# Kernel optimization log

Measured on AMD Instinct MI355X. Metric: run time of the kernel, lower is better.

The kernel has to match this reference:

```python
import jax, jax.numpy as jnp
import numpy as np

# Model constants (from module __init__ / repo script)
DT = 60                    # model time step [s]
DT_FORCING = 3600          # forcing time step [s]
NSUB = DT_FORCING // DT    # substeps between forcing samples = 60
NT = 5_040_000             # number of model steps (~9.6 years at dt=60s)
NF = NT // NSUB            # forcing series length = 84000
FC = 1e-4                  # Coriolis frequency


def setup_inputs() -> dict:
    key = jax.random.key(0)
    k1, k2, k3 = jax.random.split(key, 3)
    # pk = log(K); K ~ exp(-10) ~ 4.5e-5 keeps the Euler recurrence stable (|a|<1)
    pk = -10.0 + 0.1 * jax.random.normal(k1, (2,), dtype=jnp.float32)
    # wind stress forcing, around the repo's 0.2 N/m^2 zonal value
    TAx = 0.2 + 0.05 * jax.random.normal(k2, (NF,), dtype=jnp.float32)
    TAy = 0.05 * jax.random.normal(k3, (NF,), dtype=jnp.float32)
    return {"pk": pk, "TAx": TAx, "TAy": TAy}


def reference(pk, TAx, TAy):
    K = jnp.exp(pk)                                    # K[0]: wind coeff, K[1]: damping
    TA = TAx.astype(jnp.complex64) + 1j * TAy.astype(jnp.complex64)  # [NF]

    # Vectorized linear interpolation of forcing onto every model step it=0..NT-2
    it = jnp.arange(NT - 1)
    itf = it // NSUB
    aa = (it % NSUB).astype(jnp.float32) / NSUB
    # faithful to original: compares against NT (never true), then relies on
    # JAX's clamping gather for the final out-of-range itf+1
    itsup = jnp.where(itf + 1 >= NT, -1, itf + 1)
    TAi = (1.0 - aa) * TA[itf] + aa * TA[itsup]        # [NT-1] complex64

    # U_{t+1} = U_t + dt*(-i*fc*U_t + K0*TA_t - K1*U_t) = a*U_t + b_t
    a = jnp.asarray(1.0 + DT * (-1j * FC - K[1]), dtype=jnp.complex64)
    b = (DT * K[0]).astype(jnp.complex64) * TAi        # [NT-1]

    def step(u, bt):
        u_next = a * u + bt
        return u_next, u_next

    u0 = jnp.zeros((), dtype=jnp.complex64)
    _, ys = jax.lax.scan(step, u0, b)                  # [NT-1]
    U = jnp.concatenate([u0[None], ys])                # [NT], U[0] = 0
    return jnp.real(U), jnp.imag(U)
```

## Files before the change

kernel.cpp:

```cpp
#include <hip/hip_runtime.h>
#include <math.h>

#define NTOT   5040000
#define NFORC  84000
#define NSUB_  60
#define NSTEPS (NTOT - 1)

#define TPB     256
#define SEGS    60
#define WIN     (TPB * SEGS)
#define WARM    4800
#define CHUNK   (WIN - WARM)
#define TILE    30
#define TSTRIDE 31

__global__ __launch_bounds__(TPB, 2)
void slab_scan_kernel(const float* __restrict__ pk,
                      const float* __restrict__ TAx,
                      const float* __restrict__ TAy,
                      float* __restrict__ out)
{
    __shared__ float2 tb[TPB * TSTRIDE];

    const int tid = threadIdx.x;
    const int blk = blockIdx.x;

    const float K0 = expf(pk[0]);
    const float K1 = expf(pk[1]);
    const float ar = 1.0f - 60.0f * K1;
    const float ai = -60.0f * 1.0e-4f;
    const float s  = 60.0f * K0;

    const int wstart = blk * CHUNK;
    const int wend   = min(wstart + CHUNK, NSTEPS);
    const int ws     = max(0, wstart - WARM);

    const int itf = ws / NSUB_ + tid;
    const int i0  = min(itf,     NFORC - 1);
    const int i1  = min(itf + 1, NFORC - 1);
    const float x0 = TAx[i0], y0 = TAy[i0];
    const float x1 = TAx[i1], y1 = TAy[i1];
    const float cinv = s * (1.0f / 60.0f);
    const float dxs  = (x1 - x0) * cinv;
    const float dys  = (y1 - y0) * cinv;
    const float b0re = s * x0;
    const float b0im = s * y0;

    float ur = 0.f, ui = 0.f;
    {
        float bre = b0re, bim = b0im;
        #pragma unroll
        for (int k = 0; k < SEGS; ++k) {
            float nr = fmaf(ar, ur, fmaf(-ai, ui, bre));
            float ni = fmaf(ar, ui, fmaf( ai, ur, bim));
            ur = nr; ui = ni;
            bre += dxs; bim += dys;
        }
    }

    float2 apow[8];
    {
        double br_ = (double)ar, bi_ = (double)ai;
        double prr = 1.0, pii = 0.0;
        int e = SEGS;
        while (e) {
            if (e & 1) { double t = prr*br_ - pii*bi_; pii = prr*bi_ + pii*br_; prr = t; }
            double t = br_*br_ - bi_*bi_; bi_ = 2.0*br_*bi_; br_ = t;
            e >>= 1;
        }
        double cr = prr, ci = pii;
        #pragma unroll
        for (int k = 0; k < 8; ++k) {
            apow[k] = make_float2((float)cr, (float)ci);
            double t = cr*cr - ci*ci; ci = 2.0*cr*ci; cr = t;
        }
    }

    float2 v = make_float2(ur, ui);
    tb[tid] = v;
    __syncthreads();
    #pragma unroll
    for (int k = 0; k < 8; ++k) {
        const int off = 1 << k;
        float2 prev = make_float2(0.f, 0.f);
        if (tid >= off) prev = tb[tid - off];
        __syncthreads();
        v.x = fmaf(apow[k].x, prev.x, fmaf(-apow[k].y, prev.y, v.x));
        v.y = fmaf(apow[k].x, prev.y, fmaf( apow[k].y, prev.x, v.y));
        tb[tid] = v;
        __syncthreads();
    }
    float usr = 0.f, usi = 0.f;
    if (tid > 0) { float2 p = tb[tid - 1]; usr = p.x; usi = p.y; }
    __syncthreads();

    ur = usr; ui = usi;
    float bre = b0re, bim = b0im;
    for (int h = 0; h < SEGS / TILE; ++h) {
        #pragma unroll
        for (int k = 0; k < TILE; ++k) {
            float nr = fmaf(ar, ur, fmaf(-ai, ui, bre));
            float ni = fmaf(ar, ui, fmaf( ai, ur, bim));
            ur = nr; ui = ni;
            bre += dxs; bim += dys;
            tb[tid * TSTRIDE + k] = make_float2(nr, ni);
        }
        __syncthreads();
        {
            int row = tid / TILE;
            int k   = tid - row * TILE;
            for (int i = 0; i < TILE; ++i) {
                float2 w = tb[row * TSTRIDE + k];
                const int o = ws + row * SEGS + h * TILE + k;
                if (o >= wstart && o < wend) {
                    out[o + 1]        = w.x;
                    out[NTOT + o + 1] = w.y;
                }
                row += 8; k += 16;
                if (k >= TILE) { k -= TILE; row += 1; }
            }
        }
        __syncthreads();
    }

    if (blk == 0 && tid == 0) { out[0] = 0.f; out[NTOT] = 0.f; }
}

extern "C" void kernel_launch(void* const* d_in, const int* in_sizes, int n_in,
                              void* d_out, int out_size, void* d_ws, size_t ws_size,
                              hipStream_t stream)
{
    const float* pk  = (const float*)d_in[0];
    const float* TAx = (const float*)d_in[1];
    const float* TAy = (const float*)d_in[2];
    float* out = (float*)d_out;

    const int nblocks = (NSTEPS + CHUNK - 1) / CHUNK;
    slab_scan_kernel<<<dim3(nblocks), dim3(TPB), 0, stream>>>(pk, TAx, TAy, out);
}
```

Measured before the change: 78.31 us.

## Compute segment sums in closed form and use wave-shuffle scan with vector stores

Replaces the first sequential 60-step pass per thread with a closed-form segment contribution (G*b0 + H*db), where G and H are computed in double precision. The block-wide LDS scan, which needed many barriers, becomes a 64-lane shuffle scan plus a small cross-wave combine. The shared-memory transpose for output is dropped in favour of direct per-thread float4 stores, and launch bounds now allow 4 blocks per CU. This removes half of the serial recurrence work and most of the LDS traffic, at the cost of per-thread double-precision setup and strided, less coalesced global writes.

```diff
diff --git a/kernel.cpp b/kernel.cpp
--- a/kernel.cpp
+++ b/kernel.cpp
@@ -3,127 +3,156 @@
 
 #define NTOT   5040000
 #define NFORC  84000
-#define NSUB_  60
 #define NSTEPS (NTOT - 1)
 
-#define TPB     256
-#define SEGS    60
-#define WIN     (TPB * SEGS)
-#define WARM    4800
-#define CHUNK   (WIN - WARM)
-#define TILE    30
-#define TSTRIDE 31
+#define TPB    256
+#define SEGS   60
+#define WIN    (TPB * SEGS)
+#define WARM   4800
+#define CHUNK  (WIN - WARM)
+#define NBLK   ((NSTEPS + CHUNK - 1) / CHUNK)
 
-__global__ __launch_bounds__(TPB, 2)
-void slab_scan_kernel(const float* __restrict__ pk,
-                      const float* __restrict__ TAx,
-                      const float* __restrict__ TAy,
-                      float* __restrict__ out)
+struct cd { double x, y; };
+__device__ __forceinline__ cd cmuld(cd a, cd b){ return {a.x*b.x - a.y*b.y, a.x*b.y + a.y*b.x}; }
+__device__ __forceinline__ cd cdivd(cd a, cd b){
+    double r = 1.0 / (b.x*b.x + b.y*b.y);
+    return {(a.x*b.x + a.y*b.y)*r, (a.y*b.x - a.x*b.y)*r};
+}
+
+__device__ __forceinline__ float2 cfma(float2 m, float2 p, float2 v) {
+    v.x = fmaf(m.x, p.x, fmaf(-m.y, p.y, v.x));
+    v.y = fmaf(m.x, p.y, fmaf( m.y, p.x, v.y));
+    return v;
+}
+__device__ __forceinline__ float2 cmulf(float2 a, float2 b){
+    return make_float2(a.x*b.x - a.y*b.y, a.x*b.y + a.y*b.x);
+}
+
+__global__ __launch_bounds__(TPB, 4)
+void slab_kernel(const float* __restrict__ pk,
+                 const float* __restrict__ TAx,
+                 const float* __restrict__ TAy,
+                 float* __restrict__ out)
 {
-    __shared__ float2 tb[TPB * TSTRIDE];
+    __shared__ float2 wk[4];
 
-    const int tid = threadIdx.x;
-    const int blk = blockIdx.x;
+    const int tid  = threadIdx.x;
+    const int lane = tid & 63;
+    const int wv   = tid >> 6;
+    const int blk  = blockIdx.x;
 
-    const float K0 = expf(pk[0]);
-    const float K1 = expf(pk[1]);
-    const float ar = 1.0f - 60.0f * K1;
-    const float ai = -60.0f * 1.0e-4f;
-    const float s  = 60.0f * K0;
+    const double K0 = exp((double)pk[0]);
+    const double K1 = exp((double)pk[1]);
+    const cd a   = {1.0 - 60.0 * K1, -60.0e-4};
+    const double s = 60.0 * K0;
+
+    cd alpha = {1.0, 0.0};
+    {
+        cd p = a; int e = SEGS;
+        while (e) { if (e & 1) alpha = cmuld(alpha, p); p = cmuld(p, p); e >>= 1; }
+    }
+    const cd am1 = {a.x - 1.0, a.y};
+    const cd G = cdivd({alpha.x - 1.0, alpha.y}, am1);
+    const cd a59 = cdivd(alpha, a);
+    const cd one_m_a = {-am1.x, -am1.y};
+    cd num = {1.0 - 60.0*a59.x + 59.0*alpha.x, -60.0*a59.y + 59.0*alpha.y};
+    const cd T = cdivd(cmuld(a, num), cmuld(one_m_a, one_m_a));
+    const cd H = {59.0*G.x - T.x, 59.0*G.y - T.y};
+
+    const float2 Gf = make_float2((float)G.x, (float)G.y);
+    const float2 Hf = make_float2((float)H.x, (float)H.y);
+    float2 apf[6];
+    float2 betaf;
+    {
+        cd p = alpha;
+        #pragma unroll
+        for (int k = 0; k < 6; ++k) { apf[k] = make_float2((float)p.x, (float)p.y); p = cmuld(p, p); }
+        betaf = make_float2((float)p.x, (float)p.y);
+    }
+    const float ar  = (float)a.x;
+    const float aii = (float)a.y;
 
     const int wstart = blk * CHUNK;
     const int wend   = min(wstart + CHUNK, NSTEPS);
     const int ws     = max(0, wstart - WARM);
+    const int seg    = ws + tid * SEGS;
 
-    const int itf = ws / NSUB_ + tid;
+    const int itf = ws / SEGS + tid;
     const int i0  = min(itf,     NFORC - 1);
     const int i1  = min(itf + 1, NFORC - 1);
     const float x0 = TAx[i0], y0 = TAy[i0];
     const float x1 = TAx[i1], y1 = TAy[i1];
-    const float cinv = s * (1.0f / 60.0f);
-    const float dxs  = (x1 - x0) * cinv;
-    const float dys  = (y1 - y0) * cinv;
-    const float b0re = s * x0;
-    const float b0im = s * y0;
+    const float sF = (float)s;
+    const float2 b0 = make_float2(sF * x0, sF * y0);
+    const float  ci = sF * (1.0f / 60.0f);
+    const float2 db = make_float2((x1 - x0) * ci, (y1 - y0) * ci);
 
-    float ur = 0.f, ui = 0.f;
-    {
-        float bre = b0re, bim = b0im;
+    float2 S = cfma(Gf, b0, cmulf(Hf, db));
+
+    #pragma unroll
+    for (int k = 0; k < 6; ++k) {
+        const int off = 1 << k;
+        float px = __shfl_up(S.x, off, 64);
+        float py = __shfl_up(S.y, off, 64);
+        if (lane < off) { px = 0.f; py = 0.f; }
+        S = cfma(apf[k], make_float2(px, py), S);
+    }
+    float ex = __shfl_up(S.x, 1, 64);
+    float ey = __shfl_up(S.y, 1, 64);
+    if (lane == 0) { ex = 0.f; ey = 0.f; }
+
+    if (lane == 63) wk[wv] = S;
+    __syncthreads();
+    float2 C = make_float2(0.f, 0.f);
+    if (wv >= 1) C = wk[0];
+    if (wv >= 2) C = cfma(betaf, C, wk[1]);
+    if (wv == 3) C = cfma(betaf, C, wk[2]);
+
+    float2 al = make_float2(1.f, 0.f);
+    #pragma unroll
+    for (int k = 0; k < 6; ++k)
+        if (lane & (1 << k)) al = cmulf(al, apf[k]);
+
+    float2 u0 = cfma(al, C, make_float2(ex, ey));
+
+    if (blk == 0 && tid == 0) { out[0] = 0.f; out[NTOT] = 0.f; }
+
+    const bool live = (seg >= wstart);
+    const int  nv   = wend - seg;
+    if (!live || nv <= 0) return;
+
+    float ur = u0.x, ui = u0.y;
+    float bre = b0.x, bim = b0.y;
+    const float dbx = db.x, dby = db.y;
+    float* __restrict__ pr = out + (seg + 1);
+    float* __restrict__ pi = out + (NTOT + seg + 1);
+
+#define STEP() do { \
+        float nr_ = fmaf(ar, ur, fmaf(-aii, ui, bre)); \
+        float ni_ = fmaf(ar, ui, fmaf( aii, ur, bim)); \
+        ur = nr_; ui = ni_; bre += dbx; bim += dby; } while (0)
+
+    if (nv >= SEGS) {
         #pragma unroll
+        for (int k = 0; k < 3; ++k) { STEP(); pr[k] = ur; pi[k] = ui; }
+        #pragma unroll
+        for (int g = 0; g < 14; ++g) {
+            float4 vr, vi;
+            STEP(); vr.x = ur; vi.x = ui;
+            STEP(); vr.y = ur; vi.y = ui;
+            STEP(); vr.z = ur; vi.z = ui;
+            STEP(); vr.w = ur; vi.w = ui;
+            *reinterpret_cast<float4*>(pr + 3 + 4*g) = vr;
+            *reinterpret_cast<float4*>(pi + 3 + 4*g) = vi;
+        }
+        STEP(); pr[59] = ur; pi[59] = ui;
+    } else {
         for (int k = 0; k < SEGS; ++k) {
-            float nr = fmaf(ar, ur, fmaf(-ai, ui, bre));
-            float ni = fmaf(ar, ui, fmaf( ai, ur, bim));
-            ur = nr; ui = ni;
-            bre += dxs; bim += dys;
+            STEP();
+            if (k < nv) { pr[k] = ur; pi[k] = ui; }
         }
     }
-
-    float2 apow[8];
-    {
-        double br_ = (double)ar, bi_ = (double)ai;
-        double prr = 1.0, pii = 0.0;
-        int e = SEGS;
-        while (e) {
-            if (e & 1) { double t = prr*br_ - pii*bi_; pii = prr*bi_ + pii*br_; prr = t; }
-            double t = br_*br_ - bi_*bi_; bi_ = 2.0*br_*bi_; br_ = t;
-            e >>= 1;
-        }
-        double cr = prr, ci = pii;
-        #pragma unroll
-        for (int k = 0; k < 8; ++k) {
-            apow[k] = make_float2((float)cr, (float)ci);
-            double t = cr*cr - ci*ci; ci = 2.0*cr*ci; cr = t;
-        }
-    }
-
-    float2 v = make_float2(ur, ui);
-    tb[tid] = v;
-    __syncthreads();
-    #pragma unroll
-    for (int k = 0; k < 8; ++k) {
-        const int off = 1 << k;
-        float2 prev = make_float2(0.f, 0.f);
-        if (tid >= off) prev = tb[tid - off];
-        __syncthreads();
-        v.x = fmaf(apow[k].x, prev.x, fmaf(-apow[k].y, prev.y, v.x));
-        v.y = fmaf(apow[k].x, prev.y, fmaf( apow[k].y, prev.x, v.y));
-        tb[tid] = v;
-        __syncthreads();
-    }
-    float usr = 0.f, usi = 0.f;
-    if (tid > 0) { float2 p = tb[tid - 1]; usr = p.x; usi = p.y; }
-    __syncthreads();
-
-    ur = usr; ui = usi;
-    float bre = b0re, bim = b0im;
-    for (int h = 0; h < SEGS / TILE; ++h) {
-        #pragma unroll
-        for (int k = 0; k < TILE; ++k) {
-            float nr = fmaf(ar, ur, fmaf(-ai, ui, bre));
-            float ni = fmaf(ar, ui, fmaf( ai, ur, bim));
-            ur = nr; ui = ni;
-            bre += dxs; bim += dys;
-            tb[tid * TSTRIDE + k] = make_float2(nr, ni);
-        }
-        __syncthreads();
-        {
-            int row = tid / TILE;
-            int k   = tid - row * TILE;
-            for (int i = 0; i < TILE; ++i) {
-                float2 w = tb[row * TSTRIDE + k];
-                const int o = ws + row * SEGS + h * TILE + k;
-                if (o >= wstart && o < wend) {
-                    out[o + 1]        = w.x;
-                    out[NTOT + o + 1] = w.y;
-                }
-                row += 8; k += 16;
-                if (k >= TILE) { k -= TILE; row += 1; }
-            }
-        }
-        __syncthreads();
-    }
-
-    if (blk == 0 && tid == 0) { out[0] = 0.f; out[NTOT] = 0.f; }
+#undef STEP
 }
 
 extern "C" void kernel_launch(void* const* d_in, const int* in_sizes, int n_in,
@@ -135,6 +164,5 @@
     const float* TAy = (const float*)d_in[2];
     float* out = (float*)d_out;
 
-    const int nblocks = (NSTEPS + CHUNK - 1) / CHUNK;
-    slab_scan_kernel<<<dim3(nblocks), dim3(TPB), 0, stream>>>(pk, TAx, TAy, out);
+    slab_kernel<<<dim3(NBLK), dim3(TPB), 0, stream>>>(pk, TAx, TAy, out);
 }
```

Result: slower. 88.89 us (+13.5%).
